# Kernel tuning notes

Measured on AMD Instinct MI355X. Metric: run time of the kernel, lower is better.

## Reference

```python
import jax, jax.numpy as jnp
import numpy as np

B, S, H = 2, 2048, 2048
NQ, NKV = 32, 8          # query heads, kv heads
G = NQ // NKV            # query groups per kv head
D = H // NQ              # head dim = 64
MAX_POS = 4096
THETA = 10000.0


def _rope_tables(position_ids):
    # freqs per the original apply_rotary_emb (interleaved pair convention)
    freqs = 1.0 / THETA ** (jnp.arange(0, D, 2)[: D // 2].astype(jnp.float32) / D)
    t = jnp.arange(MAX_POS, dtype=jnp.float32)
    ang = jnp.outer(t, freqs)                     # [MAX_POS, D/2]
    cos = jnp.take(jnp.cos(ang), position_ids, axis=0)[:, :, None, :]  # [B,S,1,D/2]
    sin = jnp.take(jnp.sin(ang), position_ids, axis=0)[:, :, None, :]
    return cos, sin


def _apply_rope(x, cos, sin):
    # x: [B,S,h,D]; pairs are interleaved (x0,x1),(x2,x3),...
    x2 = x.astype(jnp.float32).reshape(*x.shape[:-1], D // 2, 2)
    xr, xi = x2[..., 0], x2[..., 1]
    out_r = xr * cos - xi * sin
    out_i = xr * sin + xi * cos
    return jnp.stack((out_r, out_i), axis=-1).reshape(x.shape).astype(x.dtype)


def setup_inputs() -> dict:
    key = jax.random.key(0)
    ks = jax.random.split(key, 5)
    init_scale = 0.02 / np.sqrt(H)
    hidden_states = jax.random.normal(ks[0], (B, S, H), dtype=jnp.float32)
    wq = jax.random.normal(ks[1], (H, H), dtype=jnp.float32) * init_scale
    wk = jax.random.normal(ks[2], (H, H // G), dtype=jnp.float32) * init_scale
    wv = jax.random.normal(ks[3], (H, H // G), dtype=jnp.float32) * init_scale
    wo = jax.random.normal(ks[4], (H, H), dtype=jnp.float32) * init_scale
    attention_mask = jnp.ones((B, S), dtype=jnp.int32)
    position_ids = jnp.broadcast_to(jnp.arange(S, dtype=jnp.int32), (B, S))
    return dict(hidden_states=hidden_states, attention_mask=attention_mask,
                position_ids=position_ids, wq=wq, wk=wk, wv=wv, wo=wo)


def reference(hidden_states, attention_mask, position_ids, wq, wk, wv, wo):
    # projections (no bias)
    xq = (hidden_states @ wq).reshape(B, S, NQ, D)
    xk = (hidden_states @ wk).reshape(B, S, NKV, D)
    xv = (hidden_states @ wv).reshape(B, S, NKV, D)
    # GQA repeat: kv head h -> query heads h*G .. h*G+G-1 (consecutive)
    xk = jnp.repeat(xk, G, axis=2)  # [B,S,NQ,D]
    xv = jnp.repeat(xv, G, axis=2)

    cos, sin = _rope_tables(position_ids)
    xq = _apply_rope(xq, cos, sin)
    xk = _apply_rope(xk, cos, sin)

    # causal + padding mask -> additive bias
    causal = jnp.tril(jnp.ones((S, S), dtype=bool))[None, None]          # [1,1,S,S]
    pad = (attention_mask > 0)[:, None, None, :]                          # [B,1,1,S]
    combined = jnp.logical_and(causal, pad)                               # [B,1,S,S]
    neg = jnp.finfo(jnp.float32).min
    bias = jnp.where(combined, 0.0, neg).astype(jnp.float32)

    scale = 1.0 / np.sqrt(D)
    scores = jnp.einsum('bqhd,bkhd->bhqk', xq, xk).astype(jnp.float32) * scale
    scores = scores + bias
    attn = jax.nn.softmax(scores, axis=-1)                                # [B,NQ,S,S] fp32
    out = jnp.einsum('bhqk,bkhd->bqhd', attn, xv)                         # [B,S,NQ,D]
    out = out.reshape(B, S, H)
    return out @ wo
```

## Files before the change

kernel.cpp:

```cpp
#include <hip/hip_runtime.h>
#include <cstdint>

typedef __attribute__((ext_vector_type(8))) __bf16  bf8v;
typedef __attribute__((ext_vector_type(4))) float   f4v;
typedef __attribute__((ext_vector_type(2))) float   f2v;
typedef __attribute__((ext_vector_type(4))) short   s4v;
typedef __attribute__((ext_vector_type(8))) unsigned short ush8;

__device__ __forceinline__ float bf2f(unsigned short u) {
    union { unsigned u; float f; } v; v.u = ((unsigned)u) << 16; return v.f;
}
__device__ __forceinline__ unsigned short f2bf_n(float f) {
    union { __bf16 h; unsigned short s; } v; v.h = (__bf16)f; return v.s;
}
__device__ __forceinline__ unsigned pack2bf(float a, float b) {
    union { __bf16 h[2]; unsigned u; } v;
    v.h[0] = (__bf16)a; v.h[1] = (__bf16)b; return v.u;
}

#define GLDS16(gp, lp)                                                          \
    __builtin_amdgcn_global_load_lds(                                           \
        (const __attribute__((address_space(1))) void*)(uintptr_t)(gp),         \
        (__attribute__((address_space(3))) void*)(uintptr_t)(lp), 16, 0, 0)

__global__ void cast_f32_to_bf16(const float* __restrict__ in,
                                 unsigned short* __restrict__ out, int n8) {
    int i = blockIdx.x * 256 + threadIdx.x;
    if (i >= n8) return;
    float4 a = ((const float4*)in)[2 * i];
    float4 b = ((const float4*)in)[2 * i + 1];
    uint4 o;
    o.x = pack2bf(a.x, a.y);
    o.y = pack2bf(a.z, a.w);
    o.z = pack2bf(b.x, b.y);
    o.w = pack2bf(b.z, b.w);
    ((uint4*)out)[i] = o;
}

__global__ void transpose_cast(const float* __restrict__ in,
                               unsigned short* __restrict__ out, int R, int C) {
    __shared__ float t[32][33];
    int c0 = blockIdx.x * 32, r0 = blockIdx.y * 32;
    int x = threadIdx.x, y = threadIdx.y;
    #pragma unroll
    for (int i = 0; i < 32; i += 8) t[y + i][x] = in[(size_t)(r0 + y + i) * C + c0 + x];
    __syncthreads();
    #pragma unroll
    for (int i = 0; i < 32; i += 8)
        out[(size_t)(c0 + y + i) * R + r0 + x] = f2bf_n(t[x][y + i]);
}

__global__ void transpose_v_bf16(const unsigned short* __restrict__ in,
                                 unsigned short* __restrict__ out) {
    __shared__ unsigned short t[32][33];
    int c0 = blockIdx.x * 32;
    int r0 = blockIdx.y * 32;
    int x = threadIdx.x, y = threadIdx.y;
    #pragma unroll
    for (int i = 0; i < 32; i += 8)
        t[y + i][x] = in[(size_t)(r0 + y + i) * 3072 + 2560 + c0 + x];
    __syncthreads();
    #pragma unroll
    for (int i = 0; i < 32; i += 8) {
        int d   = c0 + y + i;
        int tok = r0 + x;
        int g   = (tok >> 2) & 15;
        int tp  = (tok & ~63) | (((g ^ (d & 15)) << 2)) | (tok & 3);
        out[(size_t)d * 4096 + tp] = t[x][y + i];
    }
}

__global__ void rope_strided(unsigned short* __restrict__ X,
                             const int* __restrict__ pos_ids,
                             int coloff, int stride, int nh_log2,
                             float* __restrict__ kpart) {
    int idx = blockIdx.x * 256 + threadIdx.x;
    int i   = idx & 31;
    int hh  = (idx >> 5) & ((1 << nh_log2) - 1);
    int tok = idx >> (5 + nh_log2);
    int pos = pos_ids[tok];
    float ang = (float)pos * exp2f(-0.41524101186092f * (float)i);
    float s = sinf(ang), c = cosf(ang);
    unsigned short* p = X + (size_t)tok * stride + coloff + hh * 64 + 2 * i;
    unsigned pr = *(const unsigned*)p;
    float xr = bf2f((unsigned short)(pr & 0xffff));
    float xi = bf2f((unsigned short)(pr >> 16));
    float orr = xr * c - xi * s;
    float oi  = xr * s + xi * c;
    *(unsigned*)p = pack2bf(orr, oi);
    float loc = fmaxf(fabsf(orr), fabsf(oi));
    #pragma unroll
    for (int off = 1; off < 64; off <<= 1) loc = fmaxf(loc, __shfl_xor(loc, off));
    if ((threadIdx.x & 63) == 0) kpart[blockIdx.x * 4 + (threadIdx.x >> 6)] = loc;
}

__global__ void reduce_kmax(const float* __restrict__ kpart,
                            unsigned* __restrict__ kmax_out) {
    float loc = 0.f;
    #pragma unroll
    for (int i = 0; i < 16; ++i) {
        float4 v = ((const float4*)kpart)[i * 256 + threadIdx.x];
        loc = fmaxf(loc, fmaxf(fmaxf(v.x, v.y), fmaxf(v.z, v.w)));
    }
    #pragma unroll
    for (int off = 1; off < 64; off <<= 1) loc = fmaxf(loc, __shfl_xor(loc, off));
    __shared__ float warr[4];
    if ((threadIdx.x & 63) == 0) warr[threadIdx.x >> 6] = loc;
    __syncthreads();
    if (threadIdx.x == 0)
        *kmax_out = __float_as_uint(fmaxf(fmaxf(warr[0], warr[1]),
                                          fmaxf(warr[2], warr[3])));
}

template <int OUT_BF16>
__global__ __launch_bounds__(256) void gemm_bt(const unsigned short* __restrict__ A,
                                               const unsigned short* __restrict__ Bt,
                                               void* __restrict__ Cv, int N, int K) {
    __shared__ __align__(16) unsigned short As[128 * 64];
    __shared__ __align__(16) unsigned short Bs[128 * 64];
    const int t = threadIdx.x;
    const int lane = t & 63, w = t >> 6;
    const int wr = w >> 1, wc = w & 1;
    const int lr = lane & 15, lh = lane >> 4;
    const int m0 = blockIdx.y * 128, n0 = blockIdx.x * 128;

    f4v acc[4][4];
    #pragma unroll
    for (int i = 0; i < 4; ++i)
        #pragma unroll
        for (int j = 0; j < 4; ++j) acc[i][j] = f4v{0.f, 0.f, 0.f, 0.f};

    const int o_t = t * 16;
    for (int k0 = 0; k0 < K; k0 += 64) {
        __syncthreads();
        #pragma unroll
        for (int s = 0; s < 4; ++s) {
            int o = s * 4096 + o_t;
            int row = o >> 7;
            int src = (o & 127) ^ ((row & 7) << 4);
            const unsigned short* gA = A + (size_t)(m0 + row) * K + k0 + (src >> 1);
            GLDS16(gA, As + (o >> 1));
            const unsigned short* gB = Bt + (size_t)(n0 + row) * K + k0 + (src >> 1);
            GLDS16(gB, Bs + (o >> 1));
        }
        __syncthreads();
        #pragma unroll
        for (int kk = 0; kk < 2; ++kk) {
            bf8v af[4], bfr[4];
            #pragma unroll
            for (int mi = 0; mi < 4; ++mi) {
                int row = wr * 64 + mi * 16 + lr;
                int col = (kk * 32 + lh * 8) ^ ((row & 7) << 3);
                af[mi] = *(const bf8v*)(As + row * 64 + col);
            }
            #pragma unroll
            for (int ni = 0; ni < 4; ++ni) {
                int row = wc * 64 + ni * 16 + lr;
                int col = (kk * 32 + lh * 8) ^ ((row & 7) << 3);
                bfr[ni] = *(const bf8v*)(Bs + row * 64 + col);
            }
            #pragma unroll
            for (int mi = 0; mi < 4; ++mi)
                #pragma unroll
                for (int ni = 0; ni < 4; ++ni)
                    acc[mi][ni] = __builtin_amdgcn_mfma_f32_16x16x32_bf16(
                        af[mi], bfr[ni], acc[mi][ni], 0, 0, 0);
        }
    }
    #pragma unroll
    for (int mi = 0; mi < 4; ++mi)
        #pragma unroll
        for (int ni = 0; ni < 4; ++ni)
            #pragma unroll
            for (int r = 0; r < 4; ++r) {
                int row = m0 + wr * 64 + mi * 16 + lh * 4 + r;
                int col = n0 + wc * 64 + ni * 16 + lr;
                float v = acc[mi][ni][r];
                if (OUT_BF16) ((unsigned short*)Cv)[(size_t)row * N + col] = f2bf_n(v);
                else          ((float*)Cv)[(size_t)row * N + col] = v;
            }
}

__global__ __launch_bounds__(256, 4) void flash_attn(
        const unsigned short* __restrict__ QKV,
        const unsigned short* __restrict__ VtG,
        const int* __restrict__ amask,
        const int* __restrict__ pos_ids,
        const unsigned* __restrict__ kmaxp,
        unsigned short* __restrict__ O) {
    __shared__ __align__(16) unsigned short Ks[2][64 * 64];
    __shared__ __align__(16) unsigned short Vs[2][64 * 64];

    const int t = threadIdx.x, lane = t & 63, w = t >> 6;
    const int lr = lane & 15, lh = lane >> 4;
    const int pair = blockIdx.x, h = blockIdx.y, b = blockIdx.z;
    const size_t tok0 = (size_t)b * 2048;

    const unsigned short* Kb = QKV + tok0 * 3072 + 2048 + (h >> 2) * 64;
    const unsigned short* Vb = VtG + (size_t)((h >> 2) * 64) * 4096 + tok0;
    const int* amrow = amask + b * 2048;
    const float kmax = __uint_as_float(*kmaxp);

#define STAGE(buf, kt)                                                              \
    {   _Pragma("unroll")                                                           \
        for (int s_ = 0; s_ < 2; ++s_) {                                            \
            int c_ = s_ * 256 + t;                                                  \
            int row_ = c_ >> 3;                                                     \
            int sc_ = (((c_ & 7) * 16) ^ ((row_ & 7) << 4)) >> 1;                   \
            GLDS16(Kb + (size_t)((kt) * 64 + row_) * 3072 + sc_, Ks[buf] + c_ * 8); \
            GLDS16(Vb + (size_t)row_ * 4096 + (kt) * 64 + (c_ & 7) * 8,             \
                   Vs[buf] + c_ * 8);                                               \
        }                                                                           \
    }

    const float SCL = 0.18033688011112042f;
    const s4v ones = s4v{16256, 16256, 16256, 16256};

    unsigned aliveMaskV = 0;
    {
        const int4* am4 = (const int4*)amrow;
        #pragma unroll
        for (int s = 0; s < 8; ++s) {
            int4 a = am4[s * 64 + lane];
            unsigned long long bal = __ballot(a.x && a.y && a.z && a.w);
            #pragma unroll
            for (int g = 0; g < 4; ++g)
                aliveMaskV |= (((bal >> (16 * g)) & 0xFFFFull) == 0xFFFFull)
                                  ? (1u << (4 * s + g)) : 0u;
        }
    }
    const int aliveMask = __builtin_amdgcn_readfirstlane((int)aliveMaskV);

    int vcol[4];
    #pragma unroll
    for (int kf = 0; kf < 4; ++kf) vcol[kf] = ((kf * 4 + lh) ^ lr) * 4;

    int cur = 0;
    STAGE(cur, 0);

    #pragma unroll 1
    for (int half = 0; half < 2; ++half) {
        const int qt = half ? (31 - pair) : pair;
        const int q0 = qt * 64;
        const int qloc = w * 16 + lr;

        const unsigned short* Qp = QKV + (tok0 + q0 + qloc) * 3072 + h * 64;
        union Q8 { bf8v v; unsigned short s[8]; } qa0u, qa1u;
        qa0u.v = *(const bf8v*)(Qp + lh * 8);
        qa1u.v = *(const bf8v*)(Qp + 32 + lh * 8);
        float qrmax = 0.f;
        {
            int pos = pos_ids[tok0 + q0 + qloc];
            #pragma unroll
            for (int r = 0; r < 4; ++r) {
                float i0 = (float)(lh * 4 + r);
                float ang0 = (float)pos * exp2f(-0.41524101186092f * i0);
                float sn = sinf(ang0), cs = cosf(ang0);
                float xr = bf2f(qa0u.s[2 * r]), xi = bf2f(qa0u.s[2 * r + 1]);
                float a0 = (xr * cs - xi * sn) * SCL, a1 = (xr * sn + xi * cs) * SCL;
                qa0u.s[2 * r]     = f2bf_n(a0);
                qa0u.s[2 * r + 1] = f2bf_n(a1);
                float i1 = (float)(16 + lh * 4 + r);
                float ang1 = (float)pos * exp2f(-0.41524101186092f * i1);
                float sn1 = sinf(ang1), cs1 = cosf(ang1);
                float yr = bf2f(qa1u.s[2 * r]), yi = bf2f(qa1u.s[2 * r + 1]);
                float b0 = (yr * cs1 - yi * sn1) * SCL, b1 = (yr * sn1 + yi * cs1) * SCL;
                qa1u.s[2 * r]     = f2bf_n(b0);
                qa1u.s[2 * r + 1] = f2bf_n(b1);
                qrmax = fmaxf(qrmax, fmaxf(fmaxf(fabsf(a0), fabsf(a1)),
                                           fmaxf(fabsf(b0), fabsf(b1))));
            }
        }
        const bf8v qa0 = qa0u.v, qa1 = qa1u.v;
        qrmax = fmaxf(qrmax, __shfl_xor(qrmax, 16));
        qrmax = fmaxf(qrmax, __shfl_xor(qrmax, 32));
        const bool safe = __all(64.0f * qrmax * kmax * 1.02f < 80.0f);

        f4v oacc[4];
        #pragma unroll
        for (int i = 0; i < 4; ++i) oacc[i] = f4v{0.f, 0.f, 0.f, 0.f};
        f4v lacc = f4v{0.f, 0.f, 0.f, 0.f};
        float m_ = 0.f;
        f4v sa[4];

        auto qk = [&](int curb) {
            #pragma unroll
            for (int kf = 0; kf < 4; ++kf) sa[kf] = f4v{0.f, 0.f, 0.f, 0.f};
            __builtin_amdgcn_s_setprio(1);
            #pragma unroll
            for (int kk = 0; kk < 2; ++kk) {
                bf8v qa = kk ? qa1 : qa0;
                int col = kk * 32 + lh * 8;
                #pragma unroll
                for (int kf = 0; kf < 4; ++kf) {
                    bf8v kb = *(const bf8v*)(Ks[curb] + (kf * 16 + lr) * 64 + (col ^ ((lr & 7) << 3)));
                    sa[kf] = __builtin_amdgcn_mfma_f32_16x16x32_bf16(kb, qa, sa[kf], 0, 0, 0);
                }
            }
            __builtin_amdgcn_s_setprio(0);
        };

        auto pv = [&](int curb, float pe[4][4]) {
            __builtin_amdgcn_s_setprio(1);
            #pragma unroll
            for (int kf = 0; kf < 4; ++kf) {
                union { uint2 u; s4v s; } pa;
                pa.u.x = pack2bf(pe[kf][0], pe[kf][1]);
                pa.u.y = pack2bf(pe[kf][2], pe[kf][3]);
                lacc = __builtin_amdgcn_mfma_f32_16x16x16bf16_1k(pa.s, ones, lacc, 0, 0, 0);
                #pragma unroll
                for (int df = 0; df < 4; ++df) {
                    const s4v vb = *(const s4v*)(Vs[curb] + (df * 16 + lr) * 64 + vcol[kf]);
                    oacc[df] = __builtin_amdgcn_mfma_f32_16x16x16bf16_1k(
                        pa.s, vb, oacc[df], 0, 0, 0);
                }
            }
            __builtin_amdgcn_s_setprio(0);
        };

        auto softmax_pv = [&](int curb) {
            float pe[4][4];
            if (__builtin_expect(safe, 1)) {
                #pragma unroll
                for (int kf = 0; kf < 4; ++kf)
                    #pragma unroll
                    for (int r = 0; r < 4; ++r)
                        pe[kf][r] = exp2f(sa[kf][r]);
            } else {
                #pragma unroll 1
                for (;;) {
                    #pragma unroll
                    for (int kf = 0; kf < 4; ++kf)
                        #pragma unroll
                        for (int r = 0; r < 4; ++r)
                            pe[kf][r] = exp2f(sa[kf][r] - m_);
                    f2v v0 = f2v{pe[0][0], pe[0][1]} + f2v{pe[0][2], pe[0][3]};
                    f2v v1 = f2v{pe[1][0], pe[1][1]} + f2v{pe[1][2], pe[1][3]};
                    f2v v2 = f2v{pe[2][0], pe[2][1]} + f2v{pe[2][2], pe[2][3]};
                    f2v v3 = f2v{pe[3][0], pe[3][1]} + f2v{pe[3][2], pe[3][3]};
                    f2v vv = (v0 + v1) + (v2 + v3);
                    float rs = vv[0] + vv[1];
                    rs += __shfl_xor(rs, 16);
                    rs += __shfl_xor(rs, 32);
                    if (!__any(rs > 16777216.0f)) break;
                    float t0 = fmaxf(fmaxf(sa[0][0], sa[0][1]), fmaxf(sa[0][2], sa[0][3]));
                    float t1 = fmaxf(fmaxf(sa[1][0], sa[1][1]), fmaxf(sa[1][2], sa[1][3]));
                    float t2 = fmaxf(fmaxf(sa[2][0], sa[2][1]), fmaxf(sa[2][2], sa[2][3]));
                    float t3 = fmaxf(fmaxf(sa[3][0], sa[3][1]), fmaxf(sa[3][2], sa[3][3]));
                    float mx = fmaxf(fmaxf(t0, t1), fmaxf(t2, t3));
                    mx = fmaxf(mx, __shfl_xor(mx, 16));
                    mx = fmaxf(mx, __shfl_xor(mx, 32));
                    float mn = fmaxf(m_, mx);
                    float fac = exp2f(m_ - mn);
                    m_ = mn;
                    float facr[4];
                    #pragma unroll
                    for (int r = 0; r < 4; ++r) facr[r] = __shfl(fac, lh * 4 + r);
                    lacc[0] *= facr[0]; lacc[1] *= facr[1];
                    lacc[2] *= facr[2]; lacc[3] *= facr[3];
                    #pragma unroll
                    for (int df = 0; df < 4; ++df) {
                        f4v o = oacc[df];
                        o[0] *= facr[0]; o[1] *= facr[1]; o[2] *= facr[2]; o[3] *= facr[3];
                        oacc[df] = o;
                    }
                }
            }
            pv(curb, pe);
        };

        __syncthreads();

        #pragma unroll 1
        for (int kt = 0; kt < qt; ++kt) {
            STAGE(cur ^ 1, kt + 1);
            qk(cur);
            if (!((aliveMask >> kt) & 1)) {
                #pragma unroll
                for (int kf = 0; kf < 4; ++kf) {
                    int4 aq = *(const int4*)(amrow + kt * 64 + kf * 16 + lh * 4);
                    if (aq.x == 0) sa[kf][0] = -1e30f;
                    if (aq.y == 0) sa[kf][1] = -1e30f;
                    if (aq.z == 0) sa[kf][2] = -1e30f;
                    if (aq.w == 0) sa[kf][3] = -1e30f;
                }
            }
            softmax_pv(cur);
            __syncthreads();
            cur ^= 1;
        }

        if (half == 0) STAGE(cur ^ 1, 0);
        qk(cur);
        {
            const bool tileAlive = ((aliveMask >> qt) & 1) != 0;
            if (tileAlive) {
                #pragma unroll
                for (int kf = 0; kf < 4; ++kf)
                    #pragma unroll
                    for (int r = 0; r < 4; ++r) {
                        int keyl = kf * 16 + lh * 4 + r;
                        if (keyl > qloc) sa[kf][r] = -1e30f;
                    }
            } else {
                #pragma unroll
                for (int kf = 0; kf < 4; ++kf) {
                    int4 aq = *(const int4*)(amrow + qt * 64 + kf * 16 + lh * 4);
                    #pragma unroll
                    for (int r = 0; r < 4; ++r) {
                        int keyl = kf * 16 + lh * 4 + r;
                        int am = r == 0 ? aq.x : r == 1 ? aq.y : r == 2 ? aq.z : aq.w;
                        if (am == 0 || keyl > qloc) sa[kf][r] = -1e30f;
                    }
                }
            }
        }
        softmax_pv(cur);
        __syncthreads();
        cur ^= 1;

        float invr[4];
        #pragma unroll
        for (int r = 0; r < 4; ++r) invr[r] = 1.0f / lacc[r];
        #pragma unroll
        for (int df = 0; df < 4; ++df)
            #pragma unroll
            for (int r = 0; r < 4; ++r) {
                int qg = q0 + w * 16 + lh * 4 + r;
                float v = oacc[df][r] * invr[r];
                O[(tok0 + qg) * 2048 + h * 64 + df * 16 + lr] = f2bf_n(v);
            }
    }
#undef STAGE
}

extern "C" void kernel_launch(void* const* d_in, const int* in_sizes, int n_in,
                              void* d_out, int out_size, void* d_ws, size_t ws_size,
                              hipStream_t stream) {
    const float* hs   = (const float*)d_in[0];
    const int* amask  = (const int*)d_in[1];
    const int* pos    = (const int*)d_in[2];
    const float* wq   = (const float*)d_in[3];
    const float* wk   = (const float*)d_in[4];
    const float* wv   = (const float*)d_in[5];
    const float* wo   = (const float*)d_in[6];

    char* ws = (char*)d_ws;
    unsigned short* Xb   = (unsigned short*)(ws);
    unsigned short* Wqkv = (unsigned short*)(ws + 16777216);
    unsigned short* Wot  = (unsigned short*)(ws + 29360128);
    unsigned short* AOb  = (unsigned short*)(ws + 37748736);
    unsigned* kmaxp      = (unsigned*)(ws);
    float* kpart         = (float*)(ws + 1024);

    char* ob = (char*)d_out;
    unsigned short* QKV = (unsigned short*)ob;
    unsigned short* VtG = (unsigned short*)(ob + 25165824);

    cast_f32_to_bf16<<<4096, 256, 0, stream>>>(hs, Xb, 1048576);
    transpose_cast<<<dim3(64, 64), dim3(32, 8), 0, stream>>>(wq, Wqkv, 2048, 2048);
    transpose_cast<<<dim3(16, 64), dim3(32, 8), 0, stream>>>(wk, Wqkv + 4194304, 2048, 512);
    transpose_cast<<<dim3(16, 64), dim3(32, 8), 0, stream>>>(wv, Wqkv + 5242880, 2048, 512);
    transpose_cast<<<dim3(64, 64), dim3(32, 8), 0, stream>>>(wo, Wot, 2048, 2048);

    gemm_bt<1><<<dim3(24, 32), 256, 0, stream>>>(Xb, Wqkv, (void*)QKV, 3072, 2048);

    rope_strided<<<4096, 256, 0, stream>>>(QKV, pos, 2048, 3072, 3, kpart);
    reduce_kmax<<<1, 256, 0, stream>>>(kpart, kmaxp);

    transpose_v_bf16<<<dim3(16, 128), dim3(32, 8), 0, stream>>>(QKV, VtG);

    flash_attn<<<dim3(16, 32, 2), 256, 0, stream>>>(QKV, VtG, amask, pos, kmaxp, AOb);

    gemm_bt<0><<<dim3(16, 32), 256, 0, stream>>>(AOb, Wot, d_out, 2048, 2048);
}
```

Before: 219.2 us.

## Process 128-query tiles with 512-thread blocks sharing each staged K/V tile

The flash attention kernel now uses 8 waves per block covering two adjacent 64-query tiles, so each K/V tile loaded into LDS is reused by twice as many queries. The grid is halved to match, and the key loop is unified so that the wave group for the lower query tile skips compute on the last key tile while still joining the barriers. The QK product is restructured into two dependent MFMAs per key fragment, starting from a zero accumulator. The cost is fewer blocks, fewer resident blocks per CU because of the larger block size, and idle waves on the final diagonal tile.

```diff
diff --git a/kernel.cpp b/kernel.cpp
--- a/kernel.cpp
+++ b/kernel.cpp
@@ -181,7 +181,7 @@
             }
 }
 
-__global__ __launch_bounds__(256, 4) void flash_attn(
+__global__ __launch_bounds__(512, 4) void flash_attn(
         const unsigned short* __restrict__ QKV,
         const unsigned short* __restrict__ VtG,
         const int* __restrict__ amask,
@@ -193,6 +193,7 @@
 
     const int t = threadIdx.x, lane = t & 63, w = t >> 6;
     const int lr = lane & 15, lh = lane >> 4;
+    const int qsel = w >> 2, w4 = w & 3;
     const int pair = blockIdx.x, h = blockIdx.y, b = blockIdx.z;
     const size_t tok0 = (size_t)b * 2048;
 
@@ -202,19 +203,17 @@
     const float kmax = __uint_as_float(*kmaxp);
 
 #define STAGE(buf, kt)                                                              \
-    {   _Pragma("unroll")                                                           \
-        for (int s_ = 0; s_ < 2; ++s_) {                                            \
-            int c_ = s_ * 256 + t;                                                  \
-            int row_ = c_ >> 3;                                                     \
-            int sc_ = (((c_ & 7) * 16) ^ ((row_ & 7) << 4)) >> 1;                   \
-            GLDS16(Kb + (size_t)((kt) * 64 + row_) * 3072 + sc_, Ks[buf] + c_ * 8); \
-            GLDS16(Vb + (size_t)row_ * 4096 + (kt) * 64 + (c_ & 7) * 8,             \
-                   Vs[buf] + c_ * 8);                                               \
-        }                                                                           \
+    {   int c_ = t;                                                                 \
+        int row_ = c_ >> 3;                                                         \
+        int sc_ = (((c_ & 7) * 16) ^ ((row_ & 7) << 4)) >> 1;                       \
+        GLDS16(Kb + (size_t)((kt) * 64 + row_) * 3072 + sc_, Ks[buf] + c_ * 8);     \
+        GLDS16(Vb + (size_t)row_ * 4096 + (kt) * 64 + (c_ & 7) * 8,                 \
+               Vs[buf] + c_ * 8);                                                   \
     }
 
     const float SCL = 0.18033688011112042f;
     const s4v ones = s4v{16256, 16256, 16256, 16256};
+    const f4v zf = f4v{0.f, 0.f, 0.f, 0.f};
 
     unsigned aliveMaskV = 0;
     {
@@ -240,17 +239,19 @@
 
     #pragma unroll 1
     for (int half = 0; half < 2; ++half) {
-        const int qt = half ? (31 - pair) : pair;
-        const int q0 = qt * 64;
-        const int qloc = w * 16 + lr;
-
-        const unsigned short* Qp = QKV + (tok0 + q0 + qloc) * 3072 + h * 64;
+        const int sj = half ? (15 - pair) : pair;
+        const int q0 = sj * 128;
+        const int nkv = 2 * sj + 2;
+        const int qtw = 2 * sj + qsel;
+        const int qloc = w4 * 16 + lr;
+
+        const unsigned short* Qp = QKV + (tok0 + q0 + qsel * 64 + qloc) * 3072 + h * 64;
         union Q8 { bf8v v; unsigned short s[8]; } qa0u, qa1u;
         qa0u.v = *(const bf8v*)(Qp + lh * 8);
         qa1u.v = *(const bf8v*)(Qp + 32 + lh * 8);
         float qrmax = 0.f;
         {
-            int pos = pos_ids[tok0 + q0 + qloc];
+            int pos = pos_ids[tok0 + q0 + qsel * 64 + qloc];
             #pragma unroll
             for (int r = 0; r < 4; ++r) {
                 float i0 = (float)(lh * 4 + r);
@@ -284,18 +285,15 @@
         f4v sa[4];
 
         auto qk = [&](int curb) {
-            #pragma unroll
-            for (int kf = 0; kf < 4; ++kf) sa[kf] = f4v{0.f, 0.f, 0.f, 0.f};
             __builtin_amdgcn_s_setprio(1);
             #pragma unroll
-            for (int kk = 0; kk < 2; ++kk) {
-                bf8v qa = kk ? qa1 : qa0;
-                int col = kk * 32 + lh * 8;
-                #pragma unroll
-                for (int kf = 0; kf < 4; ++kf) {
-                    bf8v kb = *(const bf8v*)(Ks[curb] + (kf * 16 + lr) * 64 + (col ^ ((lr & 7) << 3)));
-                    sa[kf] = __builtin_amdgcn_mfma_f32_16x16x32_bf16(kb, qa, sa[kf], 0, 0, 0);
-                }
+            for (int kf = 0; kf < 4; ++kf) {
+                const unsigned short* Krow = Ks[curb] + (kf * 16 + lr) * 64;
+                int swz = (lr & 7) << 3;
+                bf8v kb0 = *(const bf8v*)(Krow + ((lh * 8) ^ swz));
+                f4v s0 = __builtin_amdgcn_mfma_f32_16x16x32_bf16(kb0, qa0, zf, 0, 0, 0);
+                bf8v kb1 = *(const bf8v*)(Krow + ((32 + lh * 8) ^ swz));
+                sa[kf] = __builtin_amdgcn_mfma_f32_16x16x32_bf16(kb1, qa1, s0, 0, 0, 0);
             }
             __builtin_amdgcn_s_setprio(0);
         };
@@ -372,53 +370,50 @@
         __syncthreads();
 
         #pragma unroll 1
-        for (int kt = 0; kt < qt; ++kt) {
-            STAGE(cur ^ 1, kt + 1);
-            qk(cur);
-            if (!((aliveMask >> kt) & 1)) {
-                #pragma unroll
-                for (int kf = 0; kf < 4; ++kf) {
-                    int4 aq = *(const int4*)(amrow + kt * 64 + kf * 16 + lh * 4);
-                    if (aq.x == 0) sa[kf][0] = -1e30f;
-                    if (aq.y == 0) sa[kf][1] = -1e30f;
-                    if (aq.z == 0) sa[kf][2] = -1e30f;
-                    if (aq.w == 0) sa[kf][3] = -1e30f;
+        for (int kt = 0; kt < nkv; ++kt) {
+            if (kt + 1 < nkv) STAGE(cur ^ 1, kt + 1)
+            else if (half == 0) STAGE(cur ^ 1, 0)
+
+            if (kt <= qtw) {
+                qk(cur);
+                if (kt == qtw) {
+                    if ((aliveMask >> kt) & 1) {
+                        #pragma unroll
+                        for (int kf = 0; kf < 4; ++kf)
+                            #pragma unroll
+                            for (int r = 0; r < 4; ++r) {
+                                int keyl = kf * 16 + lh * 4 + r;
+                                if (keyl > qloc) sa[kf][r] = -1e30f;
+                            }
+                    } else {
+                        #pragma unroll
+                        for (int kf = 0; kf < 4; ++kf) {
+                            int4 aq = *(const int4*)(amrow + kt * 64 + kf * 16 + lh * 4);
+                            #pragma unroll
+                            for (int r = 0; r < 4; ++r) {
+                                int keyl = kf * 16 + lh * 4 + r;
+                                int am = r == 0 ? aq.x : r == 1 ? aq.y : r == 2 ? aq.z : aq.w;
+                                if (am == 0 || keyl > qloc) sa[kf][r] = -1e30f;
+                            }
+                        }
+                    }
+                } else if (!((aliveMask >> kt) & 1)) {
+                    #pragma unroll
+                    for (int kf = 0; kf < 4; ++kf) {
+                        int4 aq = *(const int4*)(amrow + kt * 64 + kf * 16 + lh * 4);
+                        if (aq.x == 0) sa[kf][0] = -1e30f;
+                        if (aq.y == 0) sa[kf][1] = -1e30f;
+                        if (aq.z == 0) sa[kf][2] = -1e30f;
+                        if (aq.w == 0) sa[kf][3] = -1e30f;
+                    }
                 }
-            }
-            softmax_pv(cur);
+                softmax_pv(cur);
+            }
+
             __syncthreads();
             cur ^= 1;
         }
 
-        if (half == 0) STAGE(cur ^ 1, 0);
-        qk(cur);
-        {
-            const bool tileAlive = ((aliveMask >> qt) & 1) != 0;
-            if (tileAlive) {
-                #pragma unroll
-                for (int kf = 0; kf < 4; ++kf)
-                    #pragma unroll
-                    for (int r = 0; r < 4; ++r) {
-                        int keyl = kf * 16 + lh * 4 + r;
-                        if (keyl > qloc) sa[kf][r] = -1e30f;
-                    }
-            } else {
-                #pragma unroll
-                for (int kf = 0; kf < 4; ++kf) {
-                    int4 aq = *(const int4*)(amrow + qt * 64 + kf * 16 + lh * 4);
-                    #pragma unroll
-                    for (int r = 0; r < 4; ++r) {
-                        int keyl = kf * 16 + lh * 4 + r;
-                        int am = r == 0 ? aq.x : r == 1 ? aq.y : r == 2 ? aq.z : aq.w;
-                        if (am == 0 || keyl > qloc) sa[kf][r] = -1e30f;
-                    }
-                }
-            }
-        }
-        softmax_pv(cur);
-        __syncthreads();
-        cur ^= 1;
-
         float invr[4];
         #pragma unroll
         for (int r = 0; r < 4; ++r) invr[r] = 1.0f / lacc[r];
@@ -426,7 +421,7 @@
         for (int df = 0; df < 4; ++df)
             #pragma unroll
             for (int r = 0; r < 4; ++r) {
-                int qg = q0 + w * 16 + lh * 4 + r;
+                int qg = q0 + qsel * 64 + w4 * 16 + lh * 4 + r;
                 float v = oacc[df][r] * invr[r];
                 O[(tok0 + qg) * 2048 + h * 64 + df * 16 + lr] = f2bf_n(v);
             }
@@ -470,7 +465,7 @@
 
     transpose_v_bf16<<<dim3(16, 128), dim3(32, 8), 0, stream>>>(QKV, VtG);
 
-    flash_attn<<<dim3(16, 32, 2), 256, 0, stream>>>(QKV, VtG, amask, pos, kmaxp, AOb);
+    flash_attn<<<dim3(8, 32, 2), 512, 0, stream>>>(QKV, VtG, amask, pos, kmaxp, AOb);
 
     gemm_bt<0><<<dim3(16, 32), 256, 0, stream>>>(AOb, Wot, d_out, 2048, 2048);
 }
```

Result: no change. 215.4 us (median of 2 runs) (-1.7%).

## Process two 64-row query tiles per block to reuse staged K/V tiles

Applied to the files above, without the earlier changes.

Each flash-attention block now handles a 128-row query slab as two 64-row subtiles (A and B) that share every staged K/V LDS tile, so the QK and PV MFMAs run for both subtiles from one load. This halves K/V global-to-LDS traffic and barrier count per query row, and the grid shrinks to 8 pairs along x. In exchange the block uses twice the accumulator registers, which may lower occupancy, and there are half as many blocks to fill the GPU.

```diff
diff --git a/kernel.cpp b/kernel.cpp
--- a/kernel.cpp
+++ b/kernel.cpp
@@ -215,6 +215,7 @@
 
     const float SCL = 0.18033688011112042f;
     const s4v ones = s4v{16256, 16256, 16256, 16256};
+    const f4v zf = f4v{0.f, 0.f, 0.f, 0.f};
 
     unsigned aliveMaskV = 0;
     {
@@ -240,85 +241,86 @@
 
     #pragma unroll 1
     for (int half = 0; half < 2; ++half) {
-        const int qt = half ? (31 - pair) : pair;
-        const int q0 = qt * 64;
+        const int sj = half ? (15 - pair) : pair;
+        const int q0 = sj * 128;
         const int qloc = w * 16 + lr;
 
-        const unsigned short* Qp = QKV + (tok0 + q0 + qloc) * 3072 + h * 64;
-        union Q8 { bf8v v; unsigned short s[8]; } qa0u, qa1u;
-        qa0u.v = *(const bf8v*)(Qp + lh * 8);
-        qa1u.v = *(const bf8v*)(Qp + 32 + lh * 8);
-        float qrmax = 0.f;
-        {
-            int pos = pos_ids[tok0 + q0 + qloc];
+        bf8v qaA0, qaA1, qaB0, qaB1;
+        float qmA = 0.f, qmB = 0.f;
+        auto loadrope = [&](int qrow, bf8v& o0, bf8v& o1, float& qm) {
+            const unsigned short* Qp = QKV + (tok0 + qrow) * 3072 + h * 64;
+            union Q8 { bf8v v; unsigned short s[8]; } u0, u1;
+            u0.v = *(const bf8v*)(Qp + lh * 8);
+            u1.v = *(const bf8v*)(Qp + 32 + lh * 8);
+            int pos = pos_ids[tok0 + qrow];
+            float m = 0.f;
             #pragma unroll
             for (int r = 0; r < 4; ++r) {
                 float i0 = (float)(lh * 4 + r);
                 float ang0 = (float)pos * exp2f(-0.41524101186092f * i0);
                 float sn = sinf(ang0), cs = cosf(ang0);
-                float xr = bf2f(qa0u.s[2 * r]), xi = bf2f(qa0u.s[2 * r + 1]);
+                float xr = bf2f(u0.s[2 * r]), xi = bf2f(u0.s[2 * r + 1]);
                 float a0 = (xr * cs - xi * sn) * SCL, a1 = (xr * sn + xi * cs) * SCL;
-                qa0u.s[2 * r]     = f2bf_n(a0);
-                qa0u.s[2 * r + 1] = f2bf_n(a1);
+                u0.s[2 * r]     = f2bf_n(a0);
+                u0.s[2 * r + 1] = f2bf_n(a1);
                 float i1 = (float)(16 + lh * 4 + r);
                 float ang1 = (float)pos * exp2f(-0.41524101186092f * i1);
                 float sn1 = sinf(ang1), cs1 = cosf(ang1);
-                float yr = bf2f(qa1u.s[2 * r]), yi = bf2f(qa1u.s[2 * r + 1]);
+                float yr = bf2f(u1.s[2 * r]), yi = bf2f(u1.s[2 * r + 1]);
                 float b0 = (yr * cs1 - yi * sn1) * SCL, b1 = (yr * sn1 + yi * cs1) * SCL;
-                qa1u.s[2 * r]     = f2bf_n(b0);
-                qa1u.s[2 * r + 1] = f2bf_n(b1);
-                qrmax = fmaxf(qrmax, fmaxf(fmaxf(fabsf(a0), fabsf(a1)),
-                                           fmaxf(fabsf(b0), fabsf(b1))));
-            }
-        }
-        const bf8v qa0 = qa0u.v, qa1 = qa1u.v;
+                u1.s[2 * r]     = f2bf_n(b0);
+                u1.s[2 * r + 1] = f2bf_n(b1);
+                m = fmaxf(m, fmaxf(fmaxf(fabsf(a0), fabsf(a1)),
+                                   fmaxf(fabsf(b0), fabsf(b1))));
+            }
+            o0 = u0.v; o1 = u1.v; qm = m;
+        };
+        loadrope(q0 + qloc, qaA0, qaA1, qmA);
+        loadrope(q0 + 64 + qloc, qaB0, qaB1, qmB);
+        float qrmax = fmaxf(qmA, qmB);
         qrmax = fmaxf(qrmax, __shfl_xor(qrmax, 16));
         qrmax = fmaxf(qrmax, __shfl_xor(qrmax, 32));
         const bool safe = __all(64.0f * qrmax * kmax * 1.02f < 80.0f);
 
-        f4v oacc[4];
-        #pragma unroll
-        for (int i = 0; i < 4; ++i) oacc[i] = f4v{0.f, 0.f, 0.f, 0.f};
-        f4v lacc = f4v{0.f, 0.f, 0.f, 0.f};
-        float m_ = 0.f;
-        f4v sa[4];
-
-        auto qk = [&](int curb) {
-            #pragma unroll
-            for (int kf = 0; kf < 4; ++kf) sa[kf] = f4v{0.f, 0.f, 0.f, 0.f};
+        f4v oaccA[4], oaccB[4];
+        #pragma unroll
+        for (int i = 0; i < 4; ++i) { oaccA[i] = zf; oaccB[i] = zf; }
+        f4v laccA = zf, laccB = zf;
+        float mA = 0.f, mB = 0.f;
+        f4v saA[4], saB[4];
+        uint2 paA[4], paB[4];
+
+        auto qkAB = [&](int curb) {
             __builtin_amdgcn_s_setprio(1);
             #pragma unroll
-            for (int kk = 0; kk < 2; ++kk) {
-                bf8v qa = kk ? qa1 : qa0;
-                int col = kk * 32 + lh * 8;
-                #pragma unroll
-                for (int kf = 0; kf < 4; ++kf) {
-                    bf8v kb = *(const bf8v*)(Ks[curb] + (kf * 16 + lr) * 64 + (col ^ ((lr & 7) << 3)));
-                    sa[kf] = __builtin_amdgcn_mfma_f32_16x16x32_bf16(kb, qa, sa[kf], 0, 0, 0);
-                }
+            for (int kf = 0; kf < 4; ++kf) {
+                const unsigned short* Krow = Ks[curb] + (kf * 16 + lr) * 64;
+                int swz = (lr & 7) << 3;
+                bf8v kb0 = *(const bf8v*)(Krow + ((lh * 8) ^ swz));
+                bf8v kb1 = *(const bf8v*)(Krow + ((32 + lh * 8) ^ swz));
+                f4v ta = __builtin_amdgcn_mfma_f32_16x16x32_bf16(kb0, qaA0, zf, 0, 0, 0);
+                saA[kf] = __builtin_amdgcn_mfma_f32_16x16x32_bf16(kb1, qaA1, ta, 0, 0, 0);
+                f4v tb = __builtin_amdgcn_mfma_f32_16x16x32_bf16(kb0, qaB0, zf, 0, 0, 0);
+                saB[kf] = __builtin_amdgcn_mfma_f32_16x16x32_bf16(kb1, qaB1, tb, 0, 0, 0);
             }
             __builtin_amdgcn_s_setprio(0);
         };
-
-        auto pv = [&](int curb, float pe[4][4]) {
+        auto qkB = [&](int curb) {
             __builtin_amdgcn_s_setprio(1);
             #pragma unroll
             for (int kf = 0; kf < 4; ++kf) {
-                union { uint2 u; s4v s; } pa;
-                pa.u.x = pack2bf(pe[kf][0], pe[kf][1]);
-                pa.u.y = pack2bf(pe[kf][2], pe[kf][3]);
-                lacc = __builtin_amdgcn_mfma_f32_16x16x16bf16_1k(pa.s, ones, lacc, 0, 0, 0);
-                #pragma unroll
-                for (int df = 0; df < 4; ++df) {
-                    const s4v vb = *(const s4v*)(Vs[curb] + (df * 16 + lr) * 64 + vcol[kf]);
-                    oacc[df] = __builtin_amdgcn_mfma_f32_16x16x16bf16_1k(
-                        pa.s, vb, oacc[df], 0, 0, 0);
-                }
+                const unsigned short* Krow = Ks[curb] + (kf * 16 + lr) * 64;
+                int swz = (lr & 7) << 3;
+                bf8v kb0 = *(const bf8v*)(Krow + ((lh * 8) ^ swz));
+                bf8v kb1 = *(const bf8v*)(Krow + ((32 + lh * 8) ^ swz));
+                f4v tb = __builtin_amdgcn_mfma_f32_16x16x32_bf16(kb0, qaB0, zf, 0, 0, 0);
+                saB[kf] = __builtin_amdgcn_mfma_f32_16x16x32_bf16(kb1, qaB1, tb, 0, 0, 0);
             }
             __builtin_amdgcn_s_setprio(0);
         };
 
-        auto softmax_pv = [&](int curb) {
+        auto softmax_one = [&](f4v (&sa)[4], uint2 (&pa)[4], float& m_,
+                               f4v& lacc, f4v (&oacc)[4]) {
             float pe[4][4];
             if (__builtin_expect(safe, 1)) {
                 #pragma unroll
@@ -366,69 +368,133 @@
                     }
                 }
             }
-            pv(curb, pe);
+            #pragma unroll
+            for (int kf = 0; kf < 4; ++kf) {
+                pa[kf].x = pack2bf(pe[kf][0], pe[kf][1]);
+                pa[kf].y = pack2bf(pe[kf][2], pe[kf][3]);
+            }
         };
 
+        auto pvAB = [&](int curb) {
+            __builtin_amdgcn_s_setprio(1);
+            #pragma unroll
+            for (int kf = 0; kf < 4; ++kf) {
+                union { uint2 u; s4v s; } cA, cB;
+                cA.u = paA[kf]; cB.u = paB[kf];
+                laccA = __builtin_amdgcn_mfma_f32_16x16x16bf16_1k(cA.s, ones, laccA, 0, 0, 0);
+                laccB = __builtin_amdgcn_mfma_f32_16x16x16bf16_1k(cB.s, ones, laccB, 0, 0, 0);
+                #pragma unroll
+                for (int df = 0; df < 4; ++df) {
+                    const s4v vb = *(const s4v*)(Vs[curb] + (df * 16 + lr) * 64 + vcol[kf]);
+                    oaccA[df] = __builtin_amdgcn_mfma_f32_16x16x16bf16_1k(cA.s, vb, oaccA[df], 0, 0, 0);
+                    oaccB[df] = __builtin_amdgcn_mfma_f32_16x16x16bf16_1k(cB.s, vb, oaccB[df], 0, 0, 0);
+                }
+            }
+            __builtin_amdgcn_s_setprio(0);
+        };
+        auto pvB = [&](int curb) {
+            __builtin_amdgcn_s_setprio(1);
+            #pragma unroll
+            for (int kf = 0; kf < 4; ++kf) {
+                union { uint2 u; s4v s; } cB;
+                cB.u = paB[kf];
+                laccB = __builtin_amdgcn_mfma_f32_16x16x16bf16_1k(cB.s, ones, laccB, 0, 0, 0);
+                #pragma unroll
+                for (int df = 0; df < 4; ++df) {
+                    const s4v vb = *(const s4v*)(Vs[curb] + (df * 16 + lr) * 64 + vcol[kf]);
+                    oaccB[df] = __builtin_amdgcn_mfma_f32_16x16x16bf16_1k(cB.s, vb, oaccB[df], 0, 0, 0);
+                }
+            }
+            __builtin_amdgcn_s_setprio(0);
+        };
+
         __syncthreads();
 
         #pragma unroll 1
-        for (int kt = 0; kt < qt; ++kt) {
+        for (int kt = 0; kt <= 2 * sj; ++kt) {
             STAGE(cur ^ 1, kt + 1);
-            qk(cur);
-            if (!((aliveMask >> kt) & 1)) {
+            qkAB(cur);
+            const bool alive = ((aliveMask >> kt) & 1) != 0;
+            if (kt == 2 * sj) {
+                if (alive) {
+                    #pragma unroll
+                    for (int kf = 0; kf < 4; ++kf)
+                        #pragma unroll
+                        for (int r = 0; r < 4; ++r) {
+                            int keyl = kf * 16 + lh * 4 + r;
+                            if (keyl > qloc) saA[kf][r] = -1e30f;
+                        }
+                } else {
+                    #pragma unroll
+                    for (int kf = 0; kf < 4; ++kf) {
+                        int4 aq = *(const int4*)(amrow + kt * 64 + kf * 16 + lh * 4);
+                        #pragma unroll
+                        for (int r = 0; r < 4; ++r) {
+                            int keyl = kf * 16 + lh * 4 + r;
+                            int am = r == 0 ? aq.x : r == 1 ? aq.y : r == 2 ? aq.z : aq.w;
+                            if (am == 0 || keyl > qloc) saA[kf][r] = -1e30f;
+                            if (am == 0) saB[kf][r] = -1e30f;
+                        }
+                    }
+                }
+            } else if (!alive) {
                 #pragma unroll
                 for (int kf = 0; kf < 4; ++kf) {
                     int4 aq = *(const int4*)(amrow + kt * 64 + kf * 16 + lh * 4);
-                    if (aq.x == 0) sa[kf][0] = -1e30f;
-                    if (aq.y == 0) sa[kf][1] = -1e30f;
-                    if (aq.z == 0) sa[kf][2] = -1e30f;
-                    if (aq.w == 0) sa[kf][3] = -1e30f;
+                    if (aq.x == 0) { saA[kf][0] = -1e30f; saB[kf][0] = -1e30f; }
+                    if (aq.y == 0) { saA[kf][1] = -1e30f; saB[kf][1] = -1e30f; }
+                    if (aq.z == 0) { saA[kf][2] = -1e30f; saB[kf][2] = -1e30f; }
+                    if (aq.w == 0) { saA[kf][3] = -1e30f; saB[kf][3] = -1e30f; }
                 }
             }
-            softmax_pv(cur);
+            softmax_one(saA, paA, mA, laccA, oaccA);
+            softmax_one(saB, paB, mB, laccB, oaccB);
+            pvAB(cur);
             __syncthreads();
             cur ^= 1;
         }
 
-        if (half == 0) STAGE(cur ^ 1, 0);
-        qk(cur);
         {
-            const bool tileAlive = ((aliveMask >> qt) & 1) != 0;
-            if (tileAlive) {
+            const int kt = 2 * sj + 1;
+            if (half == 0) STAGE(cur ^ 1, 0);
+            qkB(cur);
+            if ((aliveMask >> kt) & 1) {
                 #pragma unroll
                 for (int kf = 0; kf < 4; ++kf)
                     #pragma unroll
                     for (int r = 0; r < 4; ++r) {
                         int keyl = kf * 16 + lh * 4 + r;
-                        if (keyl > qloc) sa[kf][r] = -1e30f;
+                        if (keyl > qloc) saB[kf][r] = -1e30f;
                     }
             } else {
                 #pragma unroll
                 for (int kf = 0; kf < 4; ++kf) {
-                    int4 aq = *(const int4*)(amrow + qt * 64 + kf * 16 + lh * 4);
+                    int4 aq = *(const int4*)(amrow + kt * 64 + kf * 16 + lh * 4);
                     #pragma unroll
                     for (int r = 0; r < 4; ++r) {
                         int keyl = kf * 16 + lh * 4 + r;
                         int am = r == 0 ? aq.x : r == 1 ? aq.y : r == 2 ? aq.z : aq.w;
-                        if (am == 0 || keyl > qloc) sa[kf][r] = -1e30f;
+                        if (am == 0 || keyl > qloc) saB[kf][r] = -1e30f;
                     }
                 }
             }
+            softmax_one(saB, paB, mB, laccB, oaccB);
+            pvB(cur);
+            __syncthreads();
+            cur ^= 1;
         }
-        softmax_pv(cur);
-        __syncthreads();
-        cur ^= 1;
-
-        float invr[4];
-        #pragma unroll
-        for (int r = 0; r < 4; ++r) invr[r] = 1.0f / lacc[r];
+
+        float invA[4], invB[4];
+        #pragma unroll
+        for (int r = 0; r < 4; ++r) { invA[r] = 1.0f / laccA[r]; invB[r] = 1.0f / laccB[r]; }
         #pragma unroll
         for (int df = 0; df < 4; ++df)
             #pragma unroll
             for (int r = 0; r < 4; ++r) {
-                int qg = q0 + w * 16 + lh * 4 + r;
-                float v = oacc[df][r] * invr[r];
-                O[(tok0 + qg) * 2048 + h * 64 + df * 16 + lr] = f2bf_n(v);
+                int qgA = q0 + w * 16 + lh * 4 + r;
+                O[(tok0 + qgA) * 2048 + h * 64 + df * 16 + lr] = f2bf_n(oaccA[df][r] * invA[r]);
+                int qgB = q0 + 64 + w * 16 + lh * 4 + r;
+                O[(tok0 + qgB) * 2048 + h * 64 + df * 16 + lr] = f2bf_n(oaccB[df][r] * invB[r]);
             }
     }
 #undef STAGE
@@ -470,7 +536,7 @@
 
     transpose_v_bf16<<<dim3(16, 128), dim3(32, 8), 0, stream>>>(QKV, VtG);
 
-    flash_attn<<<dim3(16, 32, 2), 256, 0, stream>>>(QKV, VtG, amask, pos, kmaxp, AOb);
+    flash_attn<<<dim3(8, 32, 2), 256, 0, stream>>>(QKV, VtG, amask, pos, kmaxp, AOb);
 
     gemm_bt<0><<<dim3(16, 32), 256, 0, stream>>>(AOb, Wot, d_out, 2048, 2048);
 }
```

Result: slower. 309.0 us (+41.0%).
